# Performance work log

Measured on AMD Instinct MI355X. Metric: run time of the kernel, lower is better.

## Reference

```python
import jax, jax.numpy as jnp
import numpy as np

N, B, D, H, E = 1024, 8, 768, 8, 16384
DH = D // H
EPS = 1e-5


def setup_inputs() -> dict:
    key = jax.random.key(0)
    ks = jax.random.split(key, 12)
    s = 0.02
    return {
        "x": jax.random.normal(ks[0], (N, B, D), jnp.float32),
        "edge_index": jax.random.randint(ks[1], (B, 2, E), 0, N, jnp.int32),
        "gcn_W": jax.random.normal(ks[2], (D, D), jnp.float32) * s,
        "gcn_b": jnp.zeros((D,), jnp.float32),
        "in_proj_w": jax.random.normal(ks[3], (3 * D, D), jnp.float32) * s,
        "in_proj_b": jnp.zeros((3 * D,), jnp.float32),
        "out_proj_w": jax.random.normal(ks[4], (D, D), jnp.float32) * s,
        "out_proj_b": jnp.zeros((D,), jnp.float32),
        "gate_w": jax.random.normal(ks[5], (D, 2 * D), jnp.float32) * s,
        "gate_b": jnp.zeros((D,), jnp.float32),
        "ln_g": jnp.ones((D,), jnp.float32),
        "ln_b": jnp.zeros((D,), jnp.float32),
    }


def _gcn(xb, edge_index, gcn_W, gcn_b):
    # xb: [B, N, D] node features; edge_index: [B, 2, E]
    h = xb @ gcn_W.T  # linear first, as in PyG GCNConv
    loops = jnp.arange(N, dtype=edge_index.dtype)

    def agg(h_b, ei_b):
        src = jnp.concatenate([ei_b[0], loops])  # add self-loops
        dst = jnp.concatenate([ei_b[1], loops])
        deg = jax.ops.segment_sum(jnp.ones_like(src, h_b.dtype), dst, num_segments=N)
        dinv = jnp.where(deg > 0, jax.lax.rsqrt(deg), 0.0)
        norm = dinv[src] * dinv[dst]  # symmetric normalization
        msg = norm[:, None] * h_b[src]
        return jax.ops.segment_sum(msg, dst, num_segments=N)

    return jax.vmap(agg)(h, edge_index) + gcn_b  # [B, N, D]


def _mha(x, in_proj_w, in_proj_b, out_proj_w, out_proj_b):
    # x: [N, B, D] (seq-first, as nn.MultiheadAttention default)
    qkv = x @ in_proj_w.T + in_proj_b  # [N, B, 3D]
    q, k, v = jnp.split(qkv, 3, axis=-1)

    def heads(t):  # [N, B, D] -> [B, H, N, DH]
        return t.reshape(N, B, H, DH).transpose(1, 2, 0, 3)

    q, k, v = heads(q), heads(k), heads(v)
    scores = jnp.einsum("bhqd,bhkd->bhqk", q, k) / jnp.sqrt(jnp.float32(DH))
    attn = jax.nn.softmax(scores, axis=-1)
    ctx = jnp.einsum("bhqk,bhkd->bhqd", attn, v)  # [B, H, N, DH]
    ctx = ctx.transpose(2, 0, 1, 3).reshape(N, B, D)
    return ctx @ out_proj_w.T + out_proj_b


def _layernorm(x, g, b):
    mu = jnp.mean(x, axis=-1, keepdims=True)
    var = jnp.mean(jnp.square(x - mu), axis=-1, keepdims=True)
    return (x - mu) * jax.lax.rsqrt(var + EPS) * g + b


def reference(x, edge_index, gcn_W, gcn_b, in_proj_w, in_proj_b,
              out_proj_w, out_proj_b, gate_w, gate_b, ln_g, ln_b):
    xb = x.transpose(1, 0, 2)  # [B, N, D]
    gcn_out = _gcn(xb, edge_index, gcn_W, gcn_b).transpose(1, 0, 2)  # [N, B, D]
    attn_out = _mha(x, in_proj_w, in_proj_b, out_proj_w, out_proj_b)  # [N, B, D]
    combined = jnp.concatenate([gcn_out, attn_out], axis=-1)
    gate = jax.nn.sigmoid(combined @ gate_w.T + gate_b)
    fused = gate * gcn_out + (1.0 - gate) * attn_out
    return _layernorm(fused + x, ln_g, ln_b)
```

## Files before the change

kernel.cpp:

```cpp
#include <hip/hip_runtime.h>


typedef __attribute__((ext_vector_type(8))) short b16x8;
typedef __attribute__((ext_vector_type(4))) float f32x4;

using gu32 = __attribute__((address_space(1))) const unsigned int;
using lu32 = __attribute__((address_space(3))) unsigned int;

constexpr int N  = 1024;
constexpr int B  = 8;
constexpr int D  = 768;
constexpr int H  = 8;
constexpr int DH = 96;
constexpr int E  = 16384;
constexpr int M  = N * B;
constexpr float LN_EPS = 1e-5f;

#define DEV static __device__ __forceinline__
#define GLOAD(SRC, DST) __builtin_amdgcn_global_load_lds((gu32*)(SRC), (lu32*)(DST), 16, 0, 0)

DEV unsigned short f2b(float f) {
  unsigned u = __float_as_uint(f);
  u += 0x7fffu + ((u >> 16) & 1u);
  return (unsigned short)(u >> 16);
}
DEV float b2f(unsigned short h) { return __uint_as_float(((unsigned)h) << 16); }

constexpr int CS0 = 1572864;
constexpr int CS1 = CS0 + 147456;
constexpr int CS2 = CS1 + 442368;
constexpr int CS3 = CS2 + 147456;
constexpr int CS4 = CS3 + 294912;
__global__ void cast_all_kernel(
    const float* __restrict__ x, const float* __restrict__ gcnW,
    const float* __restrict__ ipw, const float* __restrict__ opw,
    const float* __restrict__ gw,
    unsigned short* __restrict__ xb16, unsigned short* __restrict__ wcat,
    unsigned short* __restrict__ wout, unsigned short* __restrict__ wgate) {
  const int i = blockIdx.x * 256 + threadIdx.x;
  if (i >= CS4) return;
  const float* in; unsigned short* out; int off;
  if (i < CS0)      { in = x;    out = xb16;           off = i; }
  else if (i < CS1) { in = gcnW; out = wcat;           off = i - CS0; }
  else if (i < CS2) { in = ipw;  out = wcat + 589824;  off = i - CS1; }
  else if (i < CS3) { in = opw;  out = wout;           off = i - CS2; }
  else              { in = gw;   out = wgate;          off = i - CS3; }
  float4 v = ((const float4*)in)[off];
  ushort4 o;
  o.x = f2b(v.x); o.y = f2b(v.y); o.z = f2b(v.z); o.w = f2b(v.w);
  ((ushort4*)out)[off] = o;
}

__global__ void zero_i32_kernel(int* __restrict__ p, int n) {
  int i = blockIdx.x * 256 + threadIdx.x;
  if (i < n) p[i] = 0;
}

__global__ void edge_count_kernel(const int* __restrict__ ei, int* __restrict__ cnt) {
  int i = blockIdx.x * 256 + threadIdx.x;
  int b = i >> 14, e = i & (E - 1);
  int dst = ei[(b << 15) + E + e];
  atomicAdd(&cnt[(b << 10) + dst], 1);
}

__global__ __launch_bounds__(1024) void scan_offs_kernel(
    const int* __restrict__ cnt, int* __restrict__ offs,
    int* __restrict__ cursor, float* __restrict__ dinv) {
  __shared__ int buf[1024];
  const int b = blockIdx.x, i = threadIdx.x, g = (b << 10) + i;
  const int c = cnt[g];
  buf[i] = c;
  __syncthreads();
  for (int off = 1; off < 1024; off <<= 1) {
    int t = (i >= off) ? buf[i - off] : 0;
    __syncthreads();
    buf[i] += t;
    __syncthreads();
  }
  const int excl = buf[i] - c;
  offs[g] = excl;
  cursor[g] = excl;
  dinv[g] = rsqrtf((float)(c + 1));
}

__global__ void edge_fill_kernel(const int* __restrict__ ei,
                                 int* __restrict__ cursor, int* __restrict__ elist) {
  int i = blockIdx.x * 256 + threadIdx.x;
  int b = i >> 14, e = i & (E - 1);
  int src = ei[(b << 15) + e];
  int dst = ei[(b << 15) + E + e];
  int slot = atomicAdd(&cursor[(b << 10) + dst], 1);
  elist[(b << 14) + slot] = src;
}

constexpr int EPI_FUSED = 0;
constexpr int EPI_ATTN  = 1;
constexpr int EPI_GATE  = 2;

template <int EPI, int BN, int K>
__global__ __launch_bounds__(256) void gemm_bt(
    const unsigned short* __restrict__ A, const unsigned short* __restrict__ W,
    const float* __restrict__ bias,
    void* __restrict__ p0, void* __restrict__ p1, void* __restrict__ p2,
    void* __restrict__ p3) {
  constexpr int NW = BN / 32;
  constexpr int NT = K / 32;
  __shared__ __align__(16) unsigned short sA[2][128][32];
  __shared__ __align__(16) unsigned short sB[2][BN][32];
  const int tid = threadIdx.x;
  const int lane = tid & 63, wid = tid >> 6;
  const int wm = wid >> 1, wn = wid & 1;
  const int m0 = blockIdx.y * 128, n0 = blockIdx.x * BN;
  const int l15 = lane & 15, lhi = lane >> 4;
  const int srow = lane >> 2, scol = (lane & 3) * 8;

  f32x4 acc[4][NW] = {};

  const unsigned short* pa = A + ((size_t)(m0 + wid * 32 + srow)) * K + scol;
  const unsigned short* pb = W + ((size_t)(n0 + wid * (BN / 4) + srow)) * K + scol;

  auto stage = [&](int buf) {
    GLOAD(pa,          &sA[buf][wid * 32][0]);
    GLOAD(pa + 16 * K, &sA[buf][wid * 32 + 16][0]);
    GLOAD(pb,          &sB[buf][wid * (BN / 4)][0]);
    if constexpr (BN == 128) GLOAD(pb + 16 * K, &sB[buf][wid * 32 + 16][0]);
    pa += 32; pb += 32;
  };

  stage(0);
  int cur = 0;
  for (int kt = 0; kt < NT; ++kt) {
    if (kt + 1 < NT) {
      stage(cur ^ 1);
      if constexpr (BN == 128) asm volatile("s_waitcnt vmcnt(4)" ::: "memory");
      else                     asm volatile("s_waitcnt vmcnt(3)" ::: "memory");
    } else {
      asm volatile("s_waitcnt vmcnt(0)" ::: "memory");
    }
    __builtin_amdgcn_s_barrier();
    __builtin_amdgcn_sched_barrier(0);

    b16x8 af[4], bfr[NW];
#pragma unroll
    for (int i = 0; i < 4; ++i)
      af[i] = *(const b16x8*)&sA[cur][wm * 64 + i * 16 + l15][lhi * 8];
#pragma unroll
    for (int j = 0; j < NW; ++j)
      bfr[j] = *(const b16x8*)&sB[cur][wn * (BN / 2) + j * 16 + l15][lhi * 8];
#pragma unroll
    for (int i = 0; i < 4; ++i)
#pragma unroll
      for (int j = 0; j < NW; ++j)
        acc[i][j] = __builtin_amdgcn_mfma_f32_16x16x32_bf16(af[i], bfr[j], acc[i][j], 0, 0, 0);

    __builtin_amdgcn_sched_barrier(0);
    __builtin_amdgcn_s_barrier();
    cur ^= 1;
  }

#pragma unroll
  for (int i = 0; i < 4; ++i) {
#pragma unroll
    for (int j = 0; j < NW; ++j) {
      const int c = n0 + wn * (BN / 2) + j * 16 + l15;
      float bv;
      if constexpr (EPI == EPI_FUSED) bv = (c < 768) ? 0.0f : bias[c - 768];
      else bv = bias[c];
#pragma unroll
      for (int g = 0; g < 4; ++g) {
        const int r = m0 + wm * 64 + i * 16 + lhi * 4 + g;
        float v = acc[i][j][g] + bv;
        if constexpr (EPI == EPI_FUSED) {
          const int n = r >> 3, b = r & 7;
          if (c < 768) {
            ((unsigned short*)p0)[((size_t)((b << 10) + n)) * 768 + c] = f2b(v);
          } else {
            const int cc2 = c - 768;
            const int sec = cc2 / 768, cc = cc2 - sec * 768;
            const int hd = cc / 96, dh = cc - hd * 96;
            unsigned short* dst =
                (sec == 0) ? (unsigned short*)p1
                           : (sec == 1 ? (unsigned short*)p2 : (unsigned short*)p3);
            size_t idx;
            if (sec < 2) idx = ((size_t)((b * 8 + hd) * 1024 + n)) * 96 + dh;
            else         idx = ((size_t)((b * 8 + hd) * 96 + dh)) * 1024 + n;
            dst[idx] = f2b(v);
          }
        } else if constexpr (EPI == EPI_ATTN) {
          ((unsigned short*)p0)[(size_t)r * 1536 + 768 + c] = f2b(v);
        } else {
          ((unsigned short*)p0)[(size_t)r * 768 + c] =
              f2b(1.0f / (1.0f + __expf(-v)));
        }
      }
    }
  }
}

__global__ __launch_bounds__(256) void attn_kernel(
    const unsigned short* __restrict__ qb, const unsigned short* __restrict__ kb,
    const unsigned short* __restrict__ vb, unsigned short* __restrict__ ctx) {
  __shared__ __align__(16) unsigned short sK[64][104];
  __shared__ __align__(16) unsigned short sV[96][72];
  __shared__ __align__(16) unsigned short sP[4][16][72];
  const int tid = threadIdx.x, lane = tid & 63, wid = tid >> 6;
  const int l15 = lane & 15, lhi = lane >> 4;
  const int bid = blockIdx.x;
  const int xcd = bid & 7, slot = bid >> 3;
  const int bh = xcd * 8 + (slot >> 4);
  const int q0 = (slot & 15) * 64;
  const float SCL = 0.14724445f;

  b16x8 qf[3];
  const size_t qbase = ((size_t)bh * 1024 + q0 + wid * 16 + l15) * 96 + lhi * 8;
#pragma unroll
  for (int ks = 0; ks < 3; ++ks) qf[ks] = *(const b16x8*)(qb + qbase + ks * 32);

  const int c0 = tid, c1 = 256 + tid, c2 = 512 + tid;
  const unsigned short* kp0 = kb + ((size_t)bh * 1024 + c0 / 12) * 96 + (c0 % 12) * 8;
  const unsigned short* kp1 = kb + ((size_t)bh * 1024 + c1 / 12) * 96 + (c1 % 12) * 8;
  const unsigned short* kp2 = kb + ((size_t)bh * 1024 + c2 / 12) * 96 + (c2 % 12) * 8;
  const unsigned short* vp0 = vb + ((size_t)bh * 96 + (c0 >> 3)) * 1024 + (c0 & 7) * 8;
  const unsigned short* vp1 = vb + ((size_t)bh * 96 + (c1 >> 3)) * 1024 + (c1 & 7) * 8;
  const unsigned short* vp2 = vb + ((size_t)bh * 96 + (c2 >> 3)) * 1024 + (c2 & 7) * 8;
  unsigned short* sk0 = &sK[c0 / 12][(c0 % 12) * 8];
  unsigned short* sk1 = &sK[c1 / 12][(c1 % 12) * 8];
  unsigned short* sk2 = &sK[c2 / 12][(c2 % 12) * 8];
  unsigned short* sv0 = &sV[c0 >> 3][(c0 & 7) * 8];
  unsigned short* sv1 = &sV[c1 >> 3][(c1 & 7) * 8];
  unsigned short* sv2 = &sV[c2 >> 3][(c2 & 7) * 8];

  uint4 k0 = *(const uint4*)kp0, k1 = *(const uint4*)kp1, k2 = *(const uint4*)kp2;
  uint4 v0 = *(const uint4*)vp0, v1 = *(const uint4*)vp1, v2 = *(const uint4*)vp2;

  f32x4 accO[6] = {};
  float ssum[4] = {0.f, 0.f, 0.f, 0.f};

  for (int kt = 0; kt < 16; ++kt) {
    __syncthreads();
    *(uint4*)sk0 = k0; *(uint4*)sk1 = k1; *(uint4*)sk2 = k2;
    *(uint4*)sv0 = v0; *(uint4*)sv1 = v1; *(uint4*)sv2 = v2;
    __syncthreads();
    if (kt < 15) {
      kp0 += 64 * 96; kp1 += 64 * 96; kp2 += 64 * 96;
      vp0 += 64;      vp1 += 64;      vp2 += 64;
      k0 = *(const uint4*)kp0; k1 = *(const uint4*)kp1; k2 = *(const uint4*)kp2;
      v0 = *(const uint4*)vp0; v1 = *(const uint4*)vp1; v2 = *(const uint4*)vp2;
    }

    f32x4 sf[4] = {};
#pragma unroll
    for (int f = 0; f < 4; ++f) {
#pragma unroll
      for (int ks = 0; ks < 3; ++ks) {
        b16x8 kf = *(const b16x8*)&sK[f * 16 + l15][ks * 32 + lhi * 8];
        sf[f] = __builtin_amdgcn_mfma_f32_16x16x32_bf16(qf[ks], kf, sf[f], 0, 0, 0);
      }
    }

#pragma unroll
    for (int g = 0; g < 4; ++g) {
#pragma unroll
      for (int f = 0; f < 4; ++f) {
        const float pv = exp2f(sf[f][g] * SCL);
        sP[wid][lhi * 4 + g][f * 16 + l15] = f2b(pv);
        ssum[g] += pv;
      }
    }

#pragma unroll
    for (int ks = 0; ks < 2; ++ks) {
      b16x8 pa = *(const b16x8*)&sP[wid][l15][ks * 32 + lhi * 8];
#pragma unroll
      for (int o = 0; o < 6; ++o) {
        b16x8 vf = *(const b16x8*)&sV[o * 16 + l15][ks * 32 + lhi * 8];
        accO[o] = __builtin_amdgcn_mfma_f32_16x16x32_bf16(pa, vf, accO[o], 0, 0, 0);
      }
    }
  }

#pragma unroll
  for (int g = 0; g < 4; ++g) {
#pragma unroll
    for (int msk = 1; msk < 16; msk <<= 1) ssum[g] += __shfl_xor(ssum[g], msk);
  }

  const int b = bh >> 3, hd = bh & 7;
  float rinv[4];
#pragma unroll
  for (int g = 0; g < 4; ++g) rinv[g] = 1.0f / ssum[g];
#pragma unroll
  for (int o = 0; o < 6; ++o)
#pragma unroll
    for (int g = 0; g < 4; ++g) {
      const int qrow = q0 + wid * 16 + lhi * 4 + g;
      ctx[((size_t)qrow * 8 + b) * 768 + hd * 96 + o * 16 + l15] =
          f2b(accO[o][g] * rinv[g]);
    }
}

__global__ __launch_bounds__(192) void gcn_agg_kernel(
    const unsigned short* __restrict__ h16,
    const int* __restrict__ cnt, const int* __restrict__ offs,
    const int* __restrict__ elist, const float* __restrict__ dinv,
    const float* __restrict__ gcn_b, unsigned short* __restrict__ cat16) {
  const int bn = blockIdx.x;
  const int b = bn >> 10, n = bn & 1023;
  const int d = threadIdx.x * 4;
  const float dn = dinv[bn];
  const size_t hrow = (size_t)bn * 768;
  ushort4 hv = *(const ushort4*)(h16 + hrow + d);
  float a0 = dn * dn * b2f(hv.x), a1 = dn * dn * b2f(hv.y);
  float a2 = dn * dn * b2f(hv.z), a3 = dn * dn * b2f(hv.w);
  const int st = offs[bn], cv = cnt[bn];
  const int* ep = elist + (b << 14) + st;
  int i = 0;
  for (; i + 2 <= cv; i += 2) {
    const int s0 = ep[i], s1 = ep[i + 1];
    const float nv0 = dinv[(b << 10) + s0] * dn;
    const float nv1 = dinv[(b << 10) + s1] * dn;
    const ushort4 r0 = *(const ushort4*)(h16 + ((size_t)((b << 10) + s0)) * 768 + d);
    const ushort4 r1 = *(const ushort4*)(h16 + ((size_t)((b << 10) + s1)) * 768 + d);
    a0 += nv0 * b2f(r0.x) + nv1 * b2f(r1.x);
    a1 += nv0 * b2f(r0.y) + nv1 * b2f(r1.y);
    a2 += nv0 * b2f(r0.z) + nv1 * b2f(r1.z);
    a3 += nv0 * b2f(r0.w) + nv1 * b2f(r1.w);
  }
  if (i < cv) {
    const int s0 = ep[i];
    const float nv0 = dinv[(b << 10) + s0] * dn;
    const ushort4 r0 = *(const ushort4*)(h16 + ((size_t)((b << 10) + s0)) * 768 + d);
    a0 += nv0 * b2f(r0.x); a1 += nv0 * b2f(r0.y);
    a2 += nv0 * b2f(r0.z); a3 += nv0 * b2f(r0.w);
  }
  const float4 bb = *(const float4*)(gcn_b + d);
  a0 += bb.x; a1 += bb.y; a2 += bb.z; a3 += bb.w;
  const size_t crow = ((size_t)n * 8 + b) * 1536;
  ushort4 co; co.x = f2b(a0); co.y = f2b(a1); co.z = f2b(a2); co.w = f2b(a3);
  *(ushort4*)(cat16 + crow + d) = co;
}

__global__ __launch_bounds__(192) void ln_fuse_kernel(
    const unsigned short* __restrict__ gate16,
    const unsigned short* __restrict__ cat16,
    const float* __restrict__ x,
    const float* __restrict__ lng, const float* __restrict__ lnb,
    float* __restrict__ out) {
  const int r = blockIdx.x;
  const int t = threadIdx.x, lane = t & 63, wid = t >> 6;
  const int d = t * 4;
  const size_t xrow = (size_t)r * 768;
  const size_t crow = (size_t)r * 1536;
  const ushort4 gv = *(const ushort4*)(gate16 + xrow + d);
  const ushort4 cv = *(const ushort4*)(cat16 + crow + d);
  const ushort4 av = *(const ushort4*)(cat16 + crow + 768 + d);
  const float4 xv = *(const float4*)(x + xrow + d);
  const float g0 = b2f(gv.x), g1 = b2f(gv.y), g2 = b2f(gv.z), g3 = b2f(gv.w);
  float f0 = g0 * b2f(cv.x) + (1.f - g0) * b2f(av.x) + xv.x;
  float f1 = g1 * b2f(cv.y) + (1.f - g1) * b2f(av.y) + xv.y;
  float f2 = g2 * b2f(cv.z) + (1.f - g2) * b2f(av.z) + xv.z;
  float f3 = g3 * b2f(cv.w) + (1.f - g3) * b2f(av.w) + xv.w;
  float s1 = f0 + f1 + f2 + f3;
  float s2 = f0 * f0 + f1 * f1 + f2 * f2 + f3 * f3;
#pragma unroll
  for (int msk = 1; msk < 64; msk <<= 1) {
    s1 += __shfl_xor(s1, msk);
    s2 += __shfl_xor(s2, msk);
  }
  __shared__ float p1[3], p2[3];
  if (lane == 0) { p1[wid] = s1; p2[wid] = s2; }
  __syncthreads();
  s1 = p1[0] + p1[1] + p1[2];
  s2 = p2[0] + p2[1] + p2[2];
  const float mu = s1 * (1.f / 768.f);
  float var = s2 * (1.f / 768.f) - mu * mu;
  var = fmaxf(var, 0.f);
  const float rstd = rsqrtf(var + LN_EPS);
  const float4 lg = *(const float4*)(lng + d);
  const float4 lb = *(const float4*)(lnb + d);
  float4 o;
  o.x = (f0 - mu) * rstd * lg.x + lb.x;
  o.y = (f1 - mu) * rstd * lg.y + lb.y;
  o.z = (f2 - mu) * rstd * lg.z + lb.z;
  o.w = (f3 - mu) * rstd * lg.w + lb.w;
  *(float4*)(out + xrow + d) = o;
}

extern "C" void kernel_launch(void* const* d_in, const int* in_sizes, int n_in,
                              void* d_out, int out_size, void* d_ws, size_t ws_size,
                              hipStream_t stream) {
  const float* x     = (const float*)d_in[0];
  const int*   ei    = (const int*)d_in[1];
  const float* gcnW  = (const float*)d_in[2];
  const float* gcnb  = (const float*)d_in[3];
  const float* ipw   = (const float*)d_in[4];
  const float* ipb   = (const float*)d_in[5];
  const float* opw   = (const float*)d_in[6];
  const float* opb   = (const float*)d_in[7];
  const float* gw    = (const float*)d_in[8];
  const float* gb    = (const float*)d_in[9];
  const float* lng   = (const float*)d_in[10];
  const float* lnb   = (const float*)d_in[11];
  float* out = (float*)d_out;

  char* p = (char*)d_ws;
  auto alloc = [&](size_t bytes) { void* q = p; p += (bytes + 255) & ~(size_t)255; return q; };

  unsigned short* xb16  = (unsigned short*)alloc((size_t)M * 768 * 2);
  unsigned short* wcat  = (unsigned short*)alloc((size_t)3072 * 768 * 2);
  unsigned short* wout  = (unsigned short*)alloc((size_t)768 * 768 * 2);
  unsigned short* wgate = (unsigned short*)alloc((size_t)768 * 1536 * 2);
  unsigned short* qb    = (unsigned short*)alloc((size_t)B * H * N * DH * 2);
  unsigned short* kb    = (unsigned short*)alloc((size_t)B * H * N * DH * 2);
  unsigned short* vb    = (unsigned short*)alloc((size_t)B * H * DH * N * 2);
  unsigned short* h16   = (unsigned short*)alloc((size_t)M * 768 * 2);
  unsigned short* cat16 = (unsigned short*)alloc((size_t)M * 1536 * 2);
  int* cnt    = (int*)alloc(8192 * 4);
  int* offs   = (int*)alloc(8192 * 4);
  int* cursor = (int*)alloc(8192 * 4);
  float* dinv = (float*)alloc(8192 * 4);
  int* elist  = (int*)alloc((size_t)B * E * 4);

  unsigned short* ctx16  = xb16;
  unsigned short* gate16 = qb;

  cast_all_kernel<<<(CS4 + 255) / 256, 256, 0, stream>>>(
      x, gcnW, ipw, opw, gw, xb16, wcat, wout, wgate);

  zero_i32_kernel<<<32, 256, 0, stream>>>(cnt, 8192);
  edge_count_kernel<<<(B * E) / 256, 256, 0, stream>>>(ei, cnt);
  scan_offs_kernel<<<8, 1024, 0, stream>>>(cnt, offs, cursor, dinv);
  edge_fill_kernel<<<(B * E) / 256, 256, 0, stream>>>(ei, cursor, elist);

  gemm_bt<EPI_FUSED, 128, 768><<<dim3(24, 64), 256, 0, stream>>>(
      xb16, wcat, ipb, (void*)h16, (void*)qb, (void*)kb, (void*)vb);
  attn_kernel<<<1024, 256, 0, stream>>>(qb, kb, vb, ctx16);
  gcn_agg_kernel<<<8192, 192, 0, stream>>>(h16, cnt, offs, elist, dinv, gcnb, cat16);
  gemm_bt<EPI_ATTN, 64, 768><<<dim3(12, 64), 256, 0, stream>>>(
      ctx16, wout, opb, (void*)cat16, nullptr, nullptr, nullptr);
  gemm_bt<EPI_GATE, 64, 1536><<<dim3(12, 64), 256, 0, stream>>>(
      cat16, wgate, gb, (void*)gate16, nullptr, nullptr, nullptr);

  ln_fuse_kernel<<<8192, 192, 0, stream>>>(gate16, cat16, x, lng, lnb, out);
}
```

Baseline: 263.5 us.

## Triple-buffer GEMM LDS staging and remap blocks to XCDs for L2 reuse

The GEMM K-loop moves from double to triple buffering, keeping two tiles of async global-to-LDS loads in flight with adjusted vmcnt waits. This is meant to hide more load latency behind the MFMA work. The 2D grid also becomes a 1D grid whose block ids are remapped so each XCD gets a contiguous band of M rows, improving L2 reuse of the A tiles. The cost is 1.5x the LDS per block, which may lower occupancy.

```diff
diff --git a/kernel.cpp b/kernel.cpp
--- a/kernel.cpp
+++ b/kernel.cpp
@@ -97,7 +97,7 @@
 constexpr int EPI_ATTN  = 1;
 constexpr int EPI_GATE  = 2;
 
-template <int EPI, int BN, int K>
+template <int EPI, int BN, int K, int GX, int GY>
 __global__ __launch_bounds__(256) void gemm_bt(
     const unsigned short* __restrict__ A, const unsigned short* __restrict__ W,
     const float* __restrict__ bias,
@@ -105,12 +105,17 @@
     void* __restrict__ p3) {
   constexpr int NW = BN / 32;
   constexpr int NT = K / 32;
-  __shared__ __align__(16) unsigned short sA[2][128][32];
-  __shared__ __align__(16) unsigned short sB[2][BN][32];
+  static_assert(NT >= 3, "triple buffer needs >=3 K-steps");
+  __shared__ __align__(16) unsigned short sA[3][128][32];
+  __shared__ __align__(16) unsigned short sB[3][BN][32];
   const int tid = threadIdx.x;
   const int lane = tid & 63, wid = tid >> 6;
   const int wm = wid >> 1, wn = wid & 1;
-  const int m0 = blockIdx.y * 128, n0 = blockIdx.x * BN;
+  const int bid = blockIdx.x;
+  const int xcd = bid & 7, slot = bid >> 3;
+  const int by = xcd * (GY / 8) + slot / GX;
+  const int bx = slot % GX;
+  const int m0 = by * 128, n0 = bx * BN;
   const int l15 = lane & 15, lhi = lane >> 4;
   const int srow = lane >> 2, scol = (lane & 3) * 8;
 
@@ -128,10 +133,14 @@
   };
 
   stage(0);
-  int cur = 0;
+  stage(1);
+  int cb = 0, rb = 2;
   for (int kt = 0; kt < NT; ++kt) {
-    if (kt + 1 < NT) {
-      stage(cur ^ 1);
+    if (kt + 2 < NT) {
+      stage(rb);
+      if constexpr (BN == 128) asm volatile("s_waitcnt vmcnt(8)" ::: "memory");
+      else                     asm volatile("s_waitcnt vmcnt(6)" ::: "memory");
+    } else if (kt + 2 == NT) {
       if constexpr (BN == 128) asm volatile("s_waitcnt vmcnt(4)" ::: "memory");
       else                     asm volatile("s_waitcnt vmcnt(3)" ::: "memory");
     } else {
@@ -143,10 +152,10 @@
     b16x8 af[4], bfr[NW];
 #pragma unroll
     for (int i = 0; i < 4; ++i)
-      af[i] = *(const b16x8*)&sA[cur][wm * 64 + i * 16 + l15][lhi * 8];
+      af[i] = *(const b16x8*)&sA[cb][wm * 64 + i * 16 + l15][lhi * 8];
 #pragma unroll
     for (int j = 0; j < NW; ++j)
-      bfr[j] = *(const b16x8*)&sB[cur][wn * (BN / 2) + j * 16 + l15][lhi * 8];
+      bfr[j] = *(const b16x8*)&sB[cb][wn * (BN / 2) + j * 16 + l15][lhi * 8];
 #pragma unroll
     for (int i = 0; i < 4; ++i)
 #pragma unroll
@@ -155,7 +164,8 @@
 
     __builtin_amdgcn_sched_barrier(0);
     __builtin_amdgcn_s_barrier();
-    cur ^= 1;
+    cb = (cb == 2) ? 0 : cb + 1;
+    rb = (rb == 2) ? 0 : rb + 1;
   }
 
 #pragma unroll
@@ -432,13 +442,13 @@
   scan_offs_kernel<<<8, 1024, 0, stream>>>(cnt, offs, cursor, dinv);
   edge_fill_kernel<<<(B * E) / 256, 256, 0, stream>>>(ei, cursor, elist);
 
-  gemm_bt<EPI_FUSED, 128, 768><<<dim3(24, 64), 256, 0, stream>>>(
+  gemm_bt<EPI_FUSED, 128, 768, 24, 64><<<1536, 256, 0, stream>>>(
       xb16, wcat, ipb, (void*)h16, (void*)qb, (void*)kb, (void*)vb);
   attn_kernel<<<1024, 256, 0, stream>>>(qb, kb, vb, ctx16);
   gcn_agg_kernel<<<8192, 192, 0, stream>>>(h16, cnt, offs, elist, dinv, gcnb, cat16);
-  gemm_bt<EPI_ATTN, 64, 768><<<dim3(12, 64), 256, 0, stream>>>(
+  gemm_bt<EPI_ATTN, 64, 768, 12, 64><<<768, 256, 0, stream>>>(
       ctx16, wout, opb, (void*)cat16, nullptr, nullptr, nullptr);
-  gemm_bt<EPI_GATE, 64, 1536><<<dim3(12, 64), 256, 0, stream>>>(
+  gemm_bt<EPI_GATE, 64, 1536, 12, 64><<<768, 256, 0, stream>>>(
       cat16, wgate, gb, (void*)gate16, nullptr, nullptr, nullptr);
 
   ln_fuse_kernel<<<8192, 192, 0, stream>>>(gate16, cat16, x, lng, lnb, out);
```

New measurement: 256.7 us. 2.6% less time.
